# Kernel tuning notes

Hardware: AMD Instinct MI355X
Metric: run time of the kernel (lower is better)

The kernel has to match this reference:

```python
import jax, jax.numpy as jnp
import numpy as np


def _made_masks(D, H):
    # Standard MADE masks, natural ordering, param_count=2 (shift, log_scale).
    d_in = np.arange(1, D + 1)                      # input degrees 1..D
    d_h = (np.arange(H) % (D - 1)) + 1              # hidden degrees cycle 1..D-1
    d_out = np.tile(d_in, 2)                        # output degrees, 2 params per dim
    M1 = (d_h[None, :] >= d_in[:, None]).astype(np.float32)   # [D, H]
    M2 = (d_out[None, :] > d_h[:, None]).astype(np.float32)
    return jnp.asarray(M1), jnp.asarray(M2)


def setup_inputs() -> dict:
    key = jax.random.key(0)
    B, D, H = 4096, 1024, 4096
    k0, k1, k2 = jax.random.split(key, 3)
    z = jax.random.normal(k0, (B, D), dtype=jnp.float32)
    W1 = jax.random.normal(k1, (D, H), dtype=jnp.float32) * (1.0 / np.sqrt(D))
    b1 = jnp.zeros((H,), dtype=jnp.float32)
    # small init on output layer keeps exp(log_scale) well-conditioned
    W2 = jax.random.normal(k2, (H, 2 * D), dtype=jnp.float32) * (0.1 / np.sqrt(H))
    b2 = jnp.zeros((2 * D,), dtype=jnp.float32)
    permutation = jnp.arange(D, dtype=jnp.int32)
    return {"z": z, "W1": W1, "b1": b1, "W2": W2, "b2": b2, "permutation": permutation}


def reference(z, W1, b1, W2, b2, permutation):
    # IAR.forward_flow: permute -> MADE masked MLP -> split params -> affine transform -> inverse permute
    D = z.shape[1]
    H = W1.shape[1]
    M1, M2 = _made_masks(D, H)
    zp = z[:, permutation]                          # permute_data
    h = jax.nn.relu(zp @ (W1 * M1) + b1)            # [B, H]
    res = h @ (W2 * M2) + b2                        # [B, 2D]
    mu, log_s = res[:, :D], res[:, D:]              # res.split(dim_in, dim=1)
    x = zp * jnp.exp(log_s) + mu                    # affine transform, forward=True
    log_det = jnp.sum(log_s, axis=1)                # [B]
    inv = jnp.argsort(permutation)                  # inv_permute_data
    return x[:, inv], log_det
```

## Files before the change

### kernel.cpp

```cpp
#include <hip/hip_runtime.h>
#include <stdint.h>


typedef float   f32x4  __attribute__((ext_vector_type(4)));
typedef int     i32x4  __attribute__((ext_vector_type(4)));
typedef int     i32x8  __attribute__((ext_vector_type(8)));

__device__ __forceinline__ uint8_t f2fp8(float f) {
    int p = __builtin_amdgcn_cvt_pk_fp8_f32(f, 0.0f, 0, false);
    return (uint8_t)(p & 0xff);
}
__device__ __forceinline__ int8_t f2i8(float v, float s) {
    float q = rintf(v * s);
    q = fminf(fmaxf(q, -127.0f), 127.0f);
    return (int8_t)q;
}

#define GLD16(g, l)                                                          \
    __builtin_amdgcn_global_load_lds(                                        \
        (const __attribute__((address_space(1))) uint32_t*)(g),              \
        (__attribute__((address_space(3))) uint32_t*)(l), 16, 0, 0)

#define MFMA_MX(a, b, c)                                                     \
    __builtin_amdgcn_mfma_scale_f32_16x16x128_f8f6f4(                        \
        (a), (b), (c), 0, 0, 0, 0x7F7F7F7F, 0, 0x7F7F7F7F)

__global__ __launch_bounds__(256) void prep_k(
    const float* __restrict__ W1, int8_t* __restrict__ W1mT,
    const float* __restrict__ W2, uint8_t* __restrict__ W2mT,
    float* __restrict__ ws2p,
    const float* __restrict__ z, const int* __restrict__ perm,
    int8_t* __restrict__ zp, float* __restrict__ ld,
    int D, int H, int B) {
    const int bx  = blockIdx.x;
    const int tid = threadIdx.x;
    const int NB1 = (H / 64) * (D / 64);
    const int NB2 = (2 * D / 64) * (H / 64);

    if (bx < NB1) {
        __shared__ int8_t t[64][68];
        const int c0 = (bx % (H / 64)) * 64;
        const int r0 = (bx / (H / 64)) * 64;
        const int tx = tid & 63, ty = tid >> 6;

        const int fid = bx * 256 + tid;
        if (fid < B) ld[fid] = 0.0f;

        for (int rr = ty; rr < 64; rr += 4) {
            const int r = r0 + rr, c = c0 + tx;
            float v = W1[(size_t)r * H + c];
            t[rr][tx] = ((c % (D - 1)) >= r) ? f2i8(v, 1024.0f) : (int8_t)0;
        }
        __syncthreads();
#pragma unroll
        for (int pass = 0; pass < 2; pass++) {
            const int cc = pass * 32 + (tid >> 3);
            const int j0 = (tid & 7) * 8;
            union { int8_t b[8]; uint64_t q; } v;
#pragma unroll
            for (int j = 0; j < 8; j++) v.b[j] = t[j0 + j][cc];
            *(uint64_t*)&W1mT[(size_t)(c0 + cc) * D + r0 + j0] = v.q;
        }
    } else if (bx < NB1 + NB2) {
        __shared__ uint8_t t[64][68];
        const int idx = bx - NB1;
        const int c0 = (idx % (2 * D / 64)) * 64;
        const int r0 = (idx / (2 * D / 64)) * 64;
        const int tx = tid & 63, ty = tid >> 6;
        const bool second = (c0 >= D);
        const int cb = (c0 - D) >> 6;

        for (int rr = ty; rr < 64; rr += 4) {
            const int r = r0 + rr, c = c0 + tx;
            float v = W2[(size_t)r * 2 * D + c];
            bool keep = ((c % D) > (r % (D - 1)));
            t[rr][tx] = keep ? f2fp8(v * 256.0f) : (uint8_t)0;
            if (second) {
                float s = keep ? v : 0.0f;
#pragma unroll
                for (int o = 32; o > 0; o >>= 1) s += __shfl_down(s, o, 64);
                if (tx == 0) ws2p[(size_t)cb * H + r] = s;
            }
        }
        __syncthreads();
#pragma unroll
        for (int pass = 0; pass < 2; pass++) {
            const int cc = pass * 32 + (tid >> 3);
            const int j0 = (tid & 7) * 8;
            union { uint8_t b[8]; uint64_t q; } v;
#pragma unroll
            for (int j = 0; j < 8; j++) v.b[j] = t[j0 + j][cc];
            *(uint64_t*)&W2mT[(size_t)(c0 + cc) * H + r0 + j0] = v.q;
        }
    } else {
        const int bp = bx - NB1 - NB2;
        const int i0 = tid * 4;
        const int4 p4 = *(const int4*)(perm + i0);
#pragma unroll
        for (int rr = 0; rr < 2; rr++) {
            const int b = bp * 2 + rr;
            const float* zr = z + (size_t)b * D;
            union { int8_t b4[4]; uint32_t u; } q;
            q.b4[0] = f2i8(zr[p4.x], 32.0f);
            q.b4[1] = f2i8(zr[p4.y], 32.0f);
            q.b4[2] = f2i8(zr[p4.z], 32.0f);
            q.b4[3] = f2i8(zr[p4.w], 32.0f);
            *(uint32_t*)&zp[(size_t)b * D + i0] = q.u;
        }
    }
}

__global__ __launch_bounds__(256) void gemm1_k(
    const int8_t* __restrict__ A, const int8_t* __restrict__ Bt,
    const float* __restrict__ bias, const float* __restrict__ ws2p,
    uint8_t* __restrict__ Cout, float* __restrict__ ld,
    int M, int N, int K) {
    __shared__ __align__(16) int8_t Alds[128 * 128];
    __shared__ __align__(16) int8_t Blds[128 * 128];
    __shared__ float pdl[128];

    const int id   = blockIdx.x;
    const int xcd  = id & 7, s = id >> 3;
    const int mb   = s & 31;
    const int nb   = xcd * 4 + (s >> 5);
    const int m0   = mb * 128;
    const int n0   = nb * 128;

    const int tid  = threadIdx.x;
    const int lane = tid & 63;
    const int w    = tid >> 6;
    const int wm   = (w & 1) * 64;
    const int wn   = (w >> 1) * 64;
    const int quad = lane >> 4;
    const int l16  = lane & 15;

    i32x4 acc[4][4];
#pragma unroll
    for (int i = 0; i < 4; i++)
#pragma unroll
        for (int j = 0; j < 4; j++) acc[i][j] = (i32x4)0;

    const int8_t* Ag[4];
    const int8_t* Bg[4];
    int8_t *Al[4], *Bl[4];
#pragma unroll
    for (int k = 0; k < 4; k++) {
        const int c  = tid + k * 256;
        const int so = ((c & 7) ^ ((c >> 3) & 7)) * 16;
        Ag[k] = A + (size_t)(m0 + (c >> 3)) * K + so;
        Bg[k] = Bt + (size_t)(n0 + (c >> 3)) * K + so;
        Al[k] = &Alds[c * 16];
        Bl[k] = &Blds[c * 16];
    }

    const int sw   = l16 & 7;
    const int arow = (wm + l16) * 128;
    const int brow = (wn + l16) * 128;

    for (int kt = 0; kt < K; kt += 128) {
        __syncthreads();
#pragma unroll
        for (int k = 0; k < 4; k++) {
            GLD16(Ag[k] + kt, Al[k]);
            GLD16(Bg[k] + kt, Bl[k]);
        }
        __syncthreads();

#pragma unroll
        for (int kh = 0; kh < 2; kh++) {
            const int pc = ((kh * 4 + quad) ^ sw) * 16;
            i32x4 af[4], bfr[4];
#pragma unroll
            for (int mi = 0; mi < 4; mi++)
                af[mi] = *(const i32x4*)&Alds[arow + mi * 16 * 128 + pc];
#pragma unroll
            for (int ni = 0; ni < 4; ni++)
                bfr[ni] = *(const i32x4*)&Blds[brow + ni * 16 * 128 + pc];
#pragma unroll
            for (int mi = 0; mi < 4; mi++)
#pragma unroll
                for (int ni = 0; ni < 4; ni++)
                    acc[mi][ni] = __builtin_amdgcn_mfma_i32_16x16x64_i8(
                        af[mi], bfr[ni], acc[mi][ni], 0, 0, 0);
        }
    }

    const float inv = 1.0f / 32768.0f;
    float bv[4], wv[4];
#pragma unroll
    for (int ni = 0; ni < 4; ni++) {
        const int col = n0 + wn + ni * 16 + l16;
        bv[ni] = bias[col];
        float sv = 0.0f;
#pragma unroll
        for (int cb = 0; cb < 16; cb++) sv += ws2p[(size_t)cb * N + col];
        wv[ni] = sv;
    }
    float pd[4][4];
#pragma unroll
    for (int mi = 0; mi < 4; mi++)
#pragma unroll
        for (int r = 0; r < 4; r++) pd[mi][r] = 0.0f;

#pragma unroll
    for (int mi = 0; mi < 4; mi++) {
        const int row = m0 + wm + mi * 16 + quad * 4;
#pragma unroll
        for (int ni = 0; ni < 4; ni++) {
            const int col = n0 + wn + ni * 16 + l16;
#pragma unroll
            for (int r = 0; r < 4; r++) {
                float v = fmaxf((float)acc[mi][ni][r] * inv + bv[ni], 0.0f);
                pd[mi][r] += v * wv[ni];
                Cout[(size_t)(row + r) * N + col] = f2fp8(v);
            }
        }
    }

#pragma unroll
    for (int off = 1; off < 16; off <<= 1)
#pragma unroll
        for (int mi = 0; mi < 4; mi++)
#pragma unroll
            for (int r = 0; r < 4; r++)
                pd[mi][r] += __shfl_xor(pd[mi][r], off, 16);

    __syncthreads();
    if ((w >> 1) == 0 && l16 == 0)
#pragma unroll
        for (int mi = 0; mi < 4; mi++)
#pragma unroll
            for (int r = 0; r < 4; r++)
                pdl[wm + mi * 16 + quad * 4 + r] = pd[mi][r];
    __syncthreads();
    if ((w >> 1) == 1 && l16 == 0)
#pragma unroll
        for (int mi = 0; mi < 4; mi++)
#pragma unroll
            for (int r = 0; r < 4; r++)
                pdl[wm + mi * 16 + quad * 4 + r] += pd[mi][r];
    __syncthreads();
    if (tid < 128) atomicAdd(&ld[m0 + tid], pdl[tid]);
}

__global__ __launch_bounds__(256) void gemm2f_k(
    const uint8_t* __restrict__ A, const uint8_t* __restrict__ Bt,
    const float* __restrict__ b2, const int* __restrict__ perm,
    const float* __restrict__ z, const float* __restrict__ ld,
    float* __restrict__ out, int B, int D, int K) {
    __shared__ __align__(16) uint8_t Alds[2][128 * 128];
    __shared__ __align__(16) uint8_t Blds[2][128 * 128];
    __shared__ float red[4];

    const int id   = blockIdx.x;
    const int nb   = id & 15;
    const int s    = id >> 4;
    const int m0   = s * 128;
    const int p0   = nb * 64;

    const int tid  = threadIdx.x;
    const int lane = tid & 63;
    const int w    = tid >> 6;
    const int wm   = (w & 1) * 64;
    const int wp   = (w >> 1) * 32;
    const int quad = lane >> 4;
    const int l16  = lane & 15;

    f32x4 acc[4][4];
#pragma unroll
    for (int i = 0; i < 4; i++)
#pragma unroll
        for (int j = 0; j < 4; j++) acc[i][j] = (f32x4)0.0f;

    const uint8_t* Ag[4];
    const uint8_t* Bg[4];
    int ldso[4];
#pragma unroll
    for (int k = 0; k < 4; k++) {
        const int c  = tid + k * 256;
        const int r  = c >> 3;
        const int so = ((c & 7) ^ (r & 7)) * 16;
        Ag[k] = A + (size_t)(m0 + r) * K + so;
        const int g = (r < 64) ? (p0 + r) : (D + p0 + (r - 64));
        Bg[k] = Bt + (size_t)g * K + so;
        ldso[k] = c * 16;
    }

    const int sw   = l16 & 7;
    const int pc0  = ((quad * 2) ^ sw) * 16;
    const int pc1  = ((quad * 2 + 1) ^ sw) * 16;

#pragma unroll
    for (int k = 0; k < 4; k++) {
        GLD16(Ag[k], &Alds[0][ldso[k]]);
        GLD16(Bg[k], &Blds[0][ldso[k]]);
    }
    __syncthreads();

    int cur = 0;
    for (int kt = 0; kt < K; kt += 128) {
        const int nxt = cur ^ 1;
        if (kt + 128 < K) {
#pragma unroll
            for (int k = 0; k < 4; k++) {
                GLD16(Ag[k] + kt + 128, &Alds[nxt][ldso[k]]);
                GLD16(Bg[k] + kt + 128, &Blds[nxt][ldso[k]]);
            }
        }
        union ABu { int4 h2[2]; i32x8 v; };
        i32x8 af[4], bfr[4];
#pragma unroll
        for (int mi = 0; mi < 4; mi++) {
            ABu t;
            const int ar = (wm + mi * 16 + l16) * 128;
            t.h2[0] = *(const int4*)&Alds[cur][ar + pc0];
            t.h2[1] = *(const int4*)&Alds[cur][ar + pc1];
            af[mi] = t.v;
        }
#pragma unroll
        for (int ni = 0; ni < 4; ni++) {
            ABu t;
            const int br = ((ni >> 1) * 64 + wp + (ni & 1) * 16 + l16) * 128;
            t.h2[0] = *(const int4*)&Blds[cur][br + pc0];
            t.h2[1] = *(const int4*)&Blds[cur][br + pc1];
            bfr[ni] = t.v;
        }
#pragma unroll
        for (int mi = 0; mi < 4; mi++)
#pragma unroll
            for (int ni = 0; ni < 4; ni++)
                acc[mi][ni] = MFMA_MX(af[mi], bfr[ni], acc[mi][ni]);
        __syncthreads();
        cur = nxt;
    }

    const float inv = 1.0f / 256.0f;
    float bmu[2], bls[2];
    int   pcv[2];
#pragma unroll
    for (int ci = 0; ci < 2; ci++) {
        const int gc = p0 + wp + ci * 16 + l16;
        bmu[ci] = b2[gc];
        bls[ci] = b2[D + gc];
        pcv[ci] = perm[gc];
    }
#pragma unroll
    for (int mi = 0; mi < 4; mi++) {
        const int row0 = m0 + wm + mi * 16 + quad * 4;
#pragma unroll
        for (int ci = 0; ci < 2; ci++) {
#pragma unroll
            for (int r = 0; r < 4; r++) {
                const size_t idx = (size_t)(row0 + r) * D + pcv[ci];
                const float mu = acc[mi][ci][r] * inv + bmu[ci];
                float ls = acc[mi][ci + 2][r] * inv + bls[ci];
                ls = fminf(fmaxf(ls, -30.0f), 30.0f);
                out[idx] = z[idx] * expf(ls) + mu;
            }
        }
    }

    if (nb == 0) {
        float bs = 0.0f;
        for (int i = tid; i < D; i += 256) bs += b2[D + i];
#pragma unroll
        for (int o = 32; o > 0; o >>= 1) bs += __shfl_down(bs, o, 64);
        if ((tid & 63) == 0) red[tid >> 6] = bs;
        __syncthreads();
        if (tid < 128)
            out[(size_t)B * D + m0 + tid] =
                ld[m0 + tid] + red[0] + red[1] + red[2] + red[3];
    }
}

extern "C" void kernel_launch(void* const* d_in, const int* in_sizes, int n_in,
                              void* d_out, int out_size, void* d_ws, size_t ws_size,
                              hipStream_t stream) {
    const float* z    = (const float*)d_in[0];
    const float* W1   = (const float*)d_in[1];
    const float* b1   = (const float*)d_in[2];
    const float* W2   = (const float*)d_in[3];
    const float* b2   = (const float*)d_in[4];
    const int*   perm = (const int*)d_in[5];
    float* out = (float*)d_out;
    char*  ws  = (char*)d_ws;

    const int D = in_sizes[5];
    const int H = in_sizes[2];
    const int B = in_sizes[0] / D;

    const size_t off_h    = 0;
    const size_t off_W2mT = off_h    + (size_t)B * H;
    const size_t off_W1mT = off_W2mT + (size_t)2 * D * H;
    const size_t off_zp   = off_W1mT + (size_t)H * D;
    const size_t off_ws2  = off_zp   + (size_t)B * D;
    const size_t off_ld   = off_ws2  + (size_t)16 * H * 4;

    uint8_t* h    = (uint8_t*)(ws + off_h);
    uint8_t* W2mT = (uint8_t*)(ws + off_W2mT);
    int8_t*  W1mT = (int8_t*)(ws + off_W1mT);
    int8_t*  zp   = (int8_t*)(ws + off_zp);
    float*   ws2p = (float*)(ws + off_ws2);
    float*   ld   = (float*)(ws + off_ld);

    const int NB1 = (H / 64) * (D / 64);
    const int NB2 = (2 * D / 64) * (H / 64);
    const int NBP = B / 2;
    prep_k<<<NB1 + NB2 + NBP, 256, 0, stream>>>(
        W1, W1mT, W2, W2mT, ws2p, z, perm, zp, ld, D, H, B);

    gemm1_k<<<(H / 128) * (B / 128), 256, 0, stream>>>(
        zp, W1mT, b1, ws2p, h, ld, B, H, D);

    gemm2f_k<<<(D / 64) * (B / 128), 256, 0, stream>>>(
        h, W2mT, b2, perm, z, ld, out, B, D, H);
}
```

Before: 189.2 us.

## Enlarge gemm2 tile to 256 rows with 512 threads and triple-buffered LDS pipeline

After: 198.9 us. 1.05x slower.

```diff
diff --git a/kernel.cpp b/kernel.cpp
--- a/kernel.cpp
+++ b/kernel.cpp
@@ -243,26 +243,25 @@
     if (tid < 128) atomicAdd(&ld[m0 + tid], pdl[tid]);
 }
 
-__global__ __launch_bounds__(256) void gemm2f_k(
+__global__ __launch_bounds__(512) void gemm2f_k(
     const uint8_t* __restrict__ A, const uint8_t* __restrict__ Bt,
     const float* __restrict__ b2, const int* __restrict__ perm,
     const float* __restrict__ z, const float* __restrict__ ld,
     float* __restrict__ out, int B, int D, int K) {
-    __shared__ __align__(16) uint8_t Alds[2][128 * 128];
-    __shared__ __align__(16) uint8_t Blds[2][128 * 128];
-    __shared__ float red[4];
+    __shared__ __align__(16) uint8_t lds[3][49152];
+    __shared__ float red[8];
 
     const int id   = blockIdx.x;
     const int nb   = id & 15;
     const int s    = id >> 4;
-    const int m0   = s * 128;
+    const int m0   = s * 256;
     const int p0   = nb * 64;
 
     const int tid  = threadIdx.x;
     const int lane = tid & 63;
     const int w    = tid >> 6;
-    const int wm   = (w & 1) * 64;
-    const int wp   = (w >> 1) * 32;
+    const int wm   = (w & 3) * 64;
+    const int wp   = (w >> 2) * 32;
     const int quad = lane >> 4;
     const int l16  = lane & 15;
 
@@ -272,66 +271,77 @@
 #pragma unroll
         for (int j = 0; j < 4; j++) acc[i][j] = (f32x4)0.0f;
 
-    const uint8_t* Ag[4];
-    const uint8_t* Bg[4];
-    int ldso[4];
-#pragma unroll
-    for (int k = 0; k < 4; k++) {
-        const int c  = tid + k * 256;
-        const int r  = c >> 3;
-        const int so = ((c & 7) ^ (r & 7)) * 16;
-        Ag[k] = A + (size_t)(m0 + r) * K + so;
-        const int g = (r < 64) ? (p0 + r) : (D + p0 + (r - 64));
-        Bg[k] = Bt + (size_t)g * K + so;
-        ldso[k] = c * 16;
-    }
+    const uint8_t* Gsrc[6];
+    int ldst[6];
+#pragma unroll
+    for (int k = 0; k < 6; k++) {
+        const int cid = tid + k * 512;
+        const int r   = cid >> 3;
+        const int so  = ((cid & 7) ^ (r & 7)) * 16;
+        if (r < 256) {
+            Gsrc[k] = A + (size_t)(m0 + r) * K + so;
+        } else {
+            const int br = r - 256;
+            const int g  = (br < 64) ? (p0 + br) : (D + p0 + (br - 64));
+            Gsrc[k] = Bt + (size_t)g * K + so;
+        }
+        ldst[k] = cid * 16;
+    }
+
+#define STAGE2F(bi, kt)                                                      \
+    _Pragma("unroll")                                                        \
+    for (int k = 0; k < 6; k++) GLD16(Gsrc[k] + (kt), &lds[bi][ldst[k]]);
 
     const int sw   = l16 & 7;
     const int pc0  = ((quad * 2) ^ sw) * 16;
     const int pc1  = ((quad * 2 + 1) ^ sw) * 16;
-
-#pragma unroll
-    for (int k = 0; k < 4; k++) {
-        GLD16(Ag[k], &Alds[0][ldso[k]]);
-        GLD16(Bg[k], &Blds[0][ldso[k]]);
-    }
-    __syncthreads();
-
-    int cur = 0;
-    for (int kt = 0; kt < K; kt += 128) {
-        const int nxt = cur ^ 1;
-        if (kt + 128 < K) {
-#pragma unroll
-            for (int k = 0; k < 4; k++) {
-                GLD16(Ag[k] + kt + 128, &Alds[nxt][ldso[k]]);
-                GLD16(Bg[k] + kt + 128, &Blds[nxt][ldso[k]]);
-            }
-        }
+    int arow[4], brow[4];
+#pragma unroll
+    for (int mi = 0; mi < 4; mi++) arow[mi] = (wm + mi * 16 + l16) * 128;
+#pragma unroll
+    for (int ni = 0; ni < 4; ni++)
+        brow[ni] = 32768 + ((ni >> 1) * 64 + wp + (ni & 1) * 16 + l16) * 128;
+
+    STAGE2F(0, 0)
+    STAGE2F(1, 128)
+
+    const int NT = K / 128;
+    for (int t = 0; t < NT; ++t) {
+        if (t < NT - 1) {
+            asm volatile("s_waitcnt vmcnt(6)" ::: "memory");
+        } else {
+            asm volatile("s_waitcnt vmcnt(0)" ::: "memory");
+        }
+        __builtin_amdgcn_s_barrier();
+        const int cur = t % 3;
+        if (t + 2 < NT) {
+            const int nx = (t + 2) % 3;
+            STAGE2F(nx, (t + 2) * 128)
+        }
+        const uint8_t* buf = &lds[cur][0];
         union ABu { int4 h2[2]; i32x8 v; };
         i32x8 af[4], bfr[4];
 #pragma unroll
         for (int mi = 0; mi < 4; mi++) {
-            ABu t;
-            const int ar = (wm + mi * 16 + l16) * 128;
-            t.h2[0] = *(const int4*)&Alds[cur][ar + pc0];
-            t.h2[1] = *(const int4*)&Alds[cur][ar + pc1];
-            af[mi] = t.v;
+            ABu tt;
+            tt.h2[0] = *(const int4*)&buf[arow[mi] + pc0];
+            tt.h2[1] = *(const int4*)&buf[arow[mi] + pc1];
+            af[mi] = tt.v;
         }
 #pragma unroll
         for (int ni = 0; ni < 4; ni++) {
-            ABu t;
-            const int br = ((ni >> 1) * 64 + wp + (ni & 1) * 16 + l16) * 128;
-            t.h2[0] = *(const int4*)&Blds[cur][br + pc0];
-            t.h2[1] = *(const int4*)&Blds[cur][br + pc1];
-            bfr[ni] = t.v;
-        }
+            ABu tt;
+            tt.h2[0] = *(const int4*)&buf[brow[ni] + pc0];
+            tt.h2[1] = *(const int4*)&buf[brow[ni] + pc1];
+            bfr[ni] = tt.v;
+        }
+        __builtin_amdgcn_s_setprio(1);
 #pragma unroll
         for (int mi = 0; mi < 4; mi++)
 #pragma unroll
             for (int ni = 0; ni < 4; ni++)
                 acc[mi][ni] = MFMA_MX(af[mi], bfr[ni], acc[mi][ni]);
-        __syncthreads();
-        cur = nxt;
+        __builtin_amdgcn_s_setprio(0);
     }
 
     const float inv = 1.0f / 256.0f;
@@ -362,14 +372,17 @@
 
     if (nb == 0) {
         float bs = 0.0f;
-        for (int i = tid; i < D; i += 256) bs += b2[D + i];
+        for (int i = tid; i < D; i += 512) bs += b2[D + i];
 #pragma unroll
         for (int o = 32; o > 0; o >>= 1) bs += __shfl_down(bs, o, 64);
         if ((tid & 63) == 0) red[tid >> 6] = bs;
         __syncthreads();
-        if (tid < 128)
-            out[(size_t)B * D + m0 + tid] =
-                ld[m0 + tid] + red[0] + red[1] + red[2] + red[3];
+        if (tid < 256) {
+            float rs = 0.0f;
+#pragma unroll
+            for (int k = 0; k < 8; k++) rs += red[k];
+            out[(size_t)B * D + m0 + tid] = ld[m0 + tid] + rs;
+        }
     }
 }
 
@@ -412,6 +425,6 @@
     gemm1_k<<<(H / 128) * (B / 128), 256, 0, stream>>>(
         zp, W1mT, b1, ws2p, h, ld, B, H, D);
 
-    gemm2f_k<<<(D / 64) * (B / 128), 256, 0, stream>>>(
+    gemm2f_k<<<(B / 256) * (D / 64), 512, 0, stream>>>(
         h, W2mT, b2, perm, z, ld, out, B, D, H);
 }
```
